# Performance work log

Measured on AMD Instinct MI355X. Metric: run time of the kernel, lower is better.

## Reference

```python
import jax, jax.numpy as jnp
import numpy as np


def setup_inputs() -> dict:
    key = jax.random.key(0)
    k1, k2, k3 = jax.random.split(key, 3)
    return {
        "x": jax.random.normal(k1, (1, 64, 28, 28), dtype=jnp.float32),
        "w1": jax.random.normal(k2, (128, 32, 3, 3, 2), dtype=jnp.float32),  # weights[0]
        "w2": jax.random.normal(k3, (64, 3, 2), dtype=jnp.float32),          # weights[1]
    }


def reference(x, w1, w2):
    # Stage 1: first unfold + einsum == depthwise size-3 conv along W (pad 1),
    # producing 2 taps (k) per channel.
    xr = x.reshape(64, 28, 28)                      # (j, m=H, n=W)
    xp = jnp.pad(xr, ((0, 0), (0, 0), (1, 1)))      # zero-pad W by 1
    # t3[j, m, i, n] = xp[j, m, n + i]  (i = kernel offset 0..2)
    t3 = jnp.stack([xp[:, :, i:i + 28] for i in range(3)], axis=2)  # (64,28,3,28)
    t4 = jnp.einsum('jmin,jik->jmnk', t3, w2)       # (64,28,28,2)

    # Stage 2: pairwise channel-sum 64 -> 32
    t5 = t4.reshape(32, 2, 28, 28, 2).sum(axis=1)   # (l=32, h=28, w=28, k=2)

    # Stage 3: the two remaining unfolds + final einsum == standard 3x3 conv,
    # pad 1, in_channels = (l,k) = 64, out_channels = 128.
    inp = jnp.transpose(t5, (0, 3, 1, 2)).reshape(1, 64, 28, 28)       # NCHW, C=(l,k)
    w = jnp.transpose(w1, (0, 1, 4, 2, 3)).reshape(128, 64, 3, 3)      # OIHW, I=(l,m)
    y = jax.lax.conv_general_dilated(
        inp, w, window_strides=(1, 1), padding=((1, 1), (1, 1)),
        dimension_numbers=('NCHW', 'OIHW', 'NCHW'))
    return y  # (1, 128, 28, 28)
```

## Files before the change

### kernel.cpp

```cpp
#include <hip/hip_runtime.h>
#include <hip/hip_bf16.h>

__global__ __launch_bounds__(256, 4) void fused_kernel(
    const float* __restrict__ x,
    const float* __restrict__ w1,
    const float* __restrict__ w2,
    float* __restrict__ y)
{
    __shared__ __align__(16) float sA[64 * 148];

    const int b     = blockIdx.x;
    const int opair = b / 14;
    const int band  = b % 14;
    const int tid   = threadIdx.x;

    {
        const int c  = tid >> 2;
        const int pr = tid & 3;
        const int m  = band * 2 + pr - 1;
        float* dst = &sA[c * 148 + pr * 36];
        if (m < 0 || m > 27) {
            #pragma unroll
            for (int t = 0; t < 7; ++t)
                ((float4*)dst)[t] = make_float4(0.f, 0.f, 0.f, 0.f);
            ((float2*)dst)[14] = make_float2(0.f, 0.f);
        } else {
            const int j0 = c & ~1;
            const int k  = c & 1;
            const float* xr0 = x + (j0 * 28 + m) * 28;
            const float* xr1 = xr0 + 28 * 28;
            const float* w2p = w2 + j0 * 6 + k;
            const float wa0 = w2p[0], wa1 = w2p[2],  wa2 = w2p[4];
            const float wb0 = w2p[6], wb1 = w2p[8],  wb2 = w2p[10];

            float4 pv0 = make_float4(0.f, 0.f, 0.f, 0.f);
            float4 pv1 = make_float4(0.f, 0.f, 0.f, 0.f);
            #pragma unroll
            for (int t = 0; t < 7; ++t) {
                float4 v0 = ((const float4*)xr0)[t];
                float4 v1 = ((const float4*)xr1)[t];
                float4 o;
                o.x = wa0 * pv0.z + wa1 * pv0.w + wa2 * v0.x
                    + wb0 * pv1.z + wb1 * pv1.w + wb2 * v1.x;
                o.y = wa0 * pv0.w + wa1 * v0.x + wa2 * v0.y
                    + wb0 * pv1.w + wb1 * v1.x + wb2 * v1.y;
                o.z = wa0 * v0.x + wa1 * v0.y + wa2 * v0.z
                    + wb0 * v1.x + wb1 * v1.y + wb2 * v1.z;
                o.w = wa0 * v0.y + wa1 * v0.z + wa2 * v0.w
                    + wb0 * v1.y + wb1 * v1.z + wb2 * v1.w;
                if (t == 0) o.x = 0.f;
                ((float4*)dst)[t] = o;
                pv0 = v0; pv1 = v1;
            }
            float t28 = wa0 * pv0.z + wa1 * pv0.w
                      + wb0 * pv1.z + wb1 * pv1.w;
            ((float2*)dst)[14] = make_float2(t28, 0.f);
        }
    }
    __syncthreads();

    const int oo    = tid >> 7;
    const int r     = tid & 127;
    const int c8    = r & 7;
    const int strip = r >> 3;
    const bool act  = (strip < 14);
    const int dh    = strip / 7;
    const int st    = strip % 7;
    const int o     = opair * 2 + oo;

    float acc0 = 0.f, acc1 = 0.f, acc2 = 0.f, acc3 = 0.f;
    if (act) {
        const float* wbo = w1 + o * 576;
        #pragma unroll 2
        for (int ci = 0; ci < 8; ++ci) {
            const int c = c8 + ci * 8;
            const float* wc = wbo + (c >> 1) * 18 + (c & 1);
            const float* sa = &sA[c * 148 + st * 4];
            #pragma unroll
            for (int dy = 0; dy < 3; ++dy) {
                const float w0  = wc[dy * 6 + 0];
                const float w1v = wc[dy * 6 + 2];
                const float w2v = wc[dy * 6 + 4];
                const float* row = sa + (dh + dy) * 36;
                float4 t0 = *(const float4*)row;
                float2 t1 = *(const float2*)(row + 4);
                acc0 += w0 * t0.x + w1v * t0.y + w2v * t0.z;
                acc1 += w0 * t0.y + w1v * t0.z + w2v * t0.w;
                acc2 += w0 * t0.z + w1v * t0.w + w2v * t1.x;
                acc3 += w0 * t0.w + w1v * t1.x + w2v * t1.y;
            }
        }
    }

    #pragma unroll
    for (int m = 1; m <= 4; m <<= 1) {
        acc0 += __shfl_xor(acc0, m);
        acc1 += __shfl_xor(acc1, m);
        acc2 += __shfl_xor(acc2, m);
        acc3 += __shfl_xor(acc3, m);
    }

    if (act && c8 == 0) {
        const int R = band * 2 + dh;
        float* yp = y + (o * 28 + R) * 28 + st * 4;
        *(float4*)yp = make_float4(acc0, acc1, acc2, acc3);
    }
}

extern "C" void kernel_launch(void* const* d_in, const int* in_sizes, int n_in,
                              void* d_out, int out_size, void* d_ws, size_t ws_size,
                              hipStream_t stream) {
    const float* x  = (const float*)d_in[0];
    const float* w1 = (const float*)d_in[1];
    const float* w2 = (const float*)d_in[2];
    float* yout = (float*)d_out;

    fused_kernel<<<dim3(896), dim3(256), 0, stream>>>(x, w1, w2, yout);
}
```

Baseline: 17.34 us.

## Enlarge row band per block to four output rows and pair channel taps

Each block now computes four output rows instead of two, so the stage-1 depthwise result (6 padded rows per channel) is built once for more outputs, which cuts the redundant halo recomputation. The grid is halved to 448 blocks. In stage 2 each thread handles both k taps of a channel group l, using float2 weight loads and a 4-way shuffle reduction instead of 8-way, and every lane in the 28 active strips does useful work. Shared memory per block grows and the launch bound drops to 2 blocks per SM, which lowers occupancy and parallelism.

```diff
diff --git a/kernel.cpp b/kernel.cpp
--- a/kernel.cpp
+++ b/kernel.cpp
@@ -1,24 +1,24 @@
 #include <hip/hip_runtime.h>
 #include <hip/hip_bf16.h>
 
-__global__ __launch_bounds__(256, 4) void fused_kernel(
+__global__ __launch_bounds__(256, 2) void fused_kernel(
     const float* __restrict__ x,
     const float* __restrict__ w1,
     const float* __restrict__ w2,
     float* __restrict__ y)
 {
-    __shared__ __align__(16) float sA[64 * 148];
+    __shared__ __align__(16) float sA[64 * 220];
 
     const int b     = blockIdx.x;
-    const int opair = b / 14;
-    const int band  = b % 14;
+    const int opair = b / 7;
+    const int band  = b % 7;
     const int tid   = threadIdx.x;
 
-    {
-        const int c  = tid >> 2;
-        const int pr = tid & 3;
-        const int m  = band * 2 + pr - 1;
-        float* dst = &sA[c * 148 + pr * 36];
+    for (int task = tid; task < 384; task += 256) {
+        const int c  = task / 6;
+        const int pr = task % 6;
+        const int m  = band * 4 + pr - 1;
+        float* dst = &sA[c * 220 + pr * 36];
         if (m < 0 || m > 27) {
             #pragma unroll
             for (int t = 0; t < 7; ++t)
@@ -61,47 +61,52 @@
 
     const int oo    = tid >> 7;
     const int r     = tid & 127;
-    const int c8    = r & 7;
-    const int strip = r >> 3;
-    const bool act  = (strip < 14);
-    const int dh    = strip / 7;
-    const int st    = strip % 7;
+    const int c4    = r & 3;
+    const int strip = r >> 2;
+    const bool act  = (strip < 28);
+    const int sclp  = act ? strip : 0;
+    const int dh    = sclp / 7;
+    const int st    = sclp % 7;
     const int o     = opair * 2 + oo;
 
     float acc0 = 0.f, acc1 = 0.f, acc2 = 0.f, acc3 = 0.f;
-    if (act) {
-        const float* wbo = w1 + o * 576;
-        #pragma unroll 2
-        for (int ci = 0; ci < 8; ++ci) {
-            const int c = c8 + ci * 8;
-            const float* wc = wbo + (c >> 1) * 18 + (c & 1);
-            const float* sa = &sA[c * 148 + st * 4];
-            #pragma unroll
-            for (int dy = 0; dy < 3; ++dy) {
-                const float w0  = wc[dy * 6 + 0];
-                const float w1v = wc[dy * 6 + 2];
-                const float w2v = wc[dy * 6 + 4];
-                const float* row = sa + (dh + dy) * 36;
-                float4 t0 = *(const float4*)row;
-                float2 t1 = *(const float2*)(row + 4);
-                acc0 += w0 * t0.x + w1v * t0.y + w2v * t0.z;
-                acc1 += w0 * t0.y + w1v * t0.z + w2v * t0.w;
-                acc2 += w0 * t0.z + w1v * t0.w + w2v * t1.x;
-                acc3 += w0 * t0.w + w1v * t1.x + w2v * t1.y;
-            }
+    const float* wbo = w1 + o * 576;
+
+    #pragma unroll 2
+    for (int li = 0; li < 8; ++li) {
+        const int l = c4 + li * 4;
+        const float* w9 = wbo + l * 18;
+        const float* rowA = &sA[(2 * l) * 220 + dh * 36 + st * 4];
+        #pragma unroll
+        for (int dy = 0; dy < 3; ++dy) {
+            float2 ws0 = *(const float2*)(w9 + dy * 6 + 0);
+            float2 ws1 = *(const float2*)(w9 + dy * 6 + 2);
+            float2 ws2 = *(const float2*)(w9 + dy * 6 + 4);
+            const float* rA = rowA + dy * 36;
+            const float* rB = rA + 220;
+            float4 a  = *(const float4*)rA;
+            float2 a2 = *(const float2*)(rA + 4);
+            float4 bb = *(const float4*)rB;
+            float2 b2 = *(const float2*)(rB + 4);
+
+            acc0 += ws0.x * a.x  + ws1.x * a.y  + ws2.x * a.z
+                  + ws0.y * bb.x + ws1.y * bb.y + ws2.y * bb.z;
+            acc1 += ws0.x * a.y  + ws1.x * a.z  + ws2.x * a.w
+                  + ws0.y * bb.y + ws1.y * bb.z + ws2.y * bb.w;
+            acc2 += ws0.x * a.z  + ws1.x * a.w  + ws2.x * a2.x
+                  + ws0.y * bb.z + ws1.y * bb.w + ws2.y * b2.x;
+            acc3 += ws0.x * a.w  + ws1.x * a2.x + ws2.x * a2.y
+                  + ws0.y * bb.w + ws1.y * b2.x + ws2.y * b2.y;
         }
     }
 
-    #pragma unroll
-    for (int m = 1; m <= 4; m <<= 1) {
-        acc0 += __shfl_xor(acc0, m);
-        acc1 += __shfl_xor(acc1, m);
-        acc2 += __shfl_xor(acc2, m);
-        acc3 += __shfl_xor(acc3, m);
-    }
+    acc0 += __shfl_xor(acc0, 1); acc1 += __shfl_xor(acc1, 1);
+    acc2 += __shfl_xor(acc2, 1); acc3 += __shfl_xor(acc3, 1);
+    acc0 += __shfl_xor(acc0, 2); acc1 += __shfl_xor(acc1, 2);
+    acc2 += __shfl_xor(acc2, 2); acc3 += __shfl_xor(acc3, 2);
 
-    if (act && c8 == 0) {
-        const int R = band * 2 + dh;
+    if (act && c4 == 0) {
+        const int R = band * 4 + dh;
         float* yp = y + (o * 28 + R) * 28 + st * 4;
         *(float4*)yp = make_float4(acc0, acc1, acc2, acc3);
     }
@@ -115,5 +120,5 @@
     const float* w2 = (const float*)d_in[2];
     float* yout = (float*)d_out;
 
-    fused_kernel<<<dim3(896), dim3(256), 0, stream>>>(x, w1, w2, yout);
+    fused_kernel<<<dim3(448), dim3(256), 0, stream>>>(x, w1, w2, yout);
 }
```

After: 14.71 us. 15.1% less time.

## Enlarge row band to four, preload weights in registers, drop idle threads

Applied to the files above, without the earlier changes.

Each block now covers four output rows instead of two, using 448 threads so every thread is active (the old layout left 32 of 128 threads per output idle). Each thread preloads its 72 w1 weights into registers with vectorized loads before the stage-1 compute, instead of issuing scalar strided global loads inside the inner loop. This halves the grid, reduces redundant recomputation of halo rows in stage 1, and overlaps the weight fetch with stage 1. In exchange register pressure rises, occupancy drops and the grid has fewer blocks.

```diff
diff --git a/kernel.cpp b/kernel.cpp
--- a/kernel.cpp
+++ b/kernel.cpp
@@ -1,24 +1,45 @@
 #include <hip/hip_runtime.h>
 #include <hip/hip_bf16.h>
 
-__global__ __launch_bounds__(256, 4) void fused_kernel(
+__global__ __launch_bounds__(448, 2) void fused_kernel(
     const float* __restrict__ x,
     const float* __restrict__ w1,
     const float* __restrict__ w2,
     float* __restrict__ y)
 {
-    __shared__ __align__(16) float sA[64 * 148];
+    __shared__ __align__(16) float sA[64 * 220];
 
     const int b     = blockIdx.x;
-    const int opair = b / 14;
-    const int band  = b % 14;
+    const int opair = b / 7;
+    const int band  = b % 7;
     const int tid   = threadIdx.x;
 
+    const int l8    = tid & 7;
+    const int strip = tid >> 3;
+    const int oo    = strip / 28;
+    const int rr    = strip % 28;
+    const int dh    = rr / 7;
+    const int st    = rr % 7;
+    const int o     = opair * 2 + oo;
+
+    float wl[4][18];
     {
-        const int c  = tid >> 2;
-        const int pr = tid & 3;
-        const int m  = band * 2 + pr - 1;
-        float* dst = &sA[c * 148 + pr * 36];
+        const float* wb = w1 + o * 576 + l8 * 18;
+        #pragma unroll
+        for (int li = 0; li < 4; ++li) {
+            const float* p = wb + li * 144;
+            #pragma unroll
+            for (int t = 0; t < 4; ++t)
+                *(float4*)&wl[li][t * 4] = *(const float4*)(p + t * 4);
+            *(float2*)&wl[li][16] = *(const float2*)(p + 16);
+        }
+    }
+
+    if (tid < 384) {
+        const int c  = tid / 6;
+        const int pr = tid % 6;
+        const int m  = band * 4 + pr - 1;
+        float* dst = &sA[c * 220 + pr * 36];
         if (m < 0 || m > 27) {
             #pragma unroll
             for (int t = 0; t < 7; ++t)
@@ -39,17 +60,17 @@
             for (int t = 0; t < 7; ++t) {
                 float4 v0 = ((const float4*)xr0)[t];
                 float4 v1 = ((const float4*)xr1)[t];
-                float4 o;
-                o.x = wa0 * pv0.z + wa1 * pv0.w + wa2 * v0.x
-                    + wb0 * pv1.z + wb1 * pv1.w + wb2 * v1.x;
-                o.y = wa0 * pv0.w + wa1 * v0.x + wa2 * v0.y
-                    + wb0 * pv1.w + wb1 * v1.x + wb2 * v1.y;
-                o.z = wa0 * v0.x + wa1 * v0.y + wa2 * v0.z
-                    + wb0 * v1.x + wb1 * v1.y + wb2 * v1.z;
-                o.w = wa0 * v0.y + wa1 * v0.z + wa2 * v0.w
-                    + wb0 * v1.y + wb1 * v1.z + wb2 * v1.w;
-                if (t == 0) o.x = 0.f;
-                ((float4*)dst)[t] = o;
+                float4 ov;
+                ov.x = wa0 * pv0.z + wa1 * pv0.w + wa2 * v0.x
+                     + wb0 * pv1.z + wb1 * pv1.w + wb2 * v1.x;
+                ov.y = wa0 * pv0.w + wa1 * v0.x + wa2 * v0.y
+                     + wb0 * pv1.w + wb1 * v1.x + wb2 * v1.y;
+                ov.z = wa0 * v0.x + wa1 * v0.y + wa2 * v0.z
+                     + wb0 * v1.x + wb1 * v1.y + wb2 * v1.z;
+                ov.w = wa0 * v0.y + wa1 * v0.z + wa2 * v0.w
+                     + wb0 * v1.y + wb1 * v1.z + wb2 * v1.w;
+                if (t == 0) ov.x = 0.f;
+                ((float4*)dst)[t] = ov;
                 pv0 = v0; pv1 = v1;
             }
             float t28 = wa0 * pv0.z + wa1 * pv0.w
@@ -59,35 +80,26 @@
     }
     __syncthreads();
 
-    const int oo    = tid >> 7;
-    const int r     = tid & 127;
-    const int c8    = r & 7;
-    const int strip = r >> 3;
-    const bool act  = (strip < 14);
-    const int dh    = strip / 7;
-    const int st    = strip % 7;
-    const int o     = opair * 2 + oo;
+    float acc0 = 0.f, acc1 = 0.f, acc2 = 0.f, acc3 = 0.f;
 
-    float acc0 = 0.f, acc1 = 0.f, acc2 = 0.f, acc3 = 0.f;
-    if (act) {
-        const float* wbo = w1 + o * 576;
-        #pragma unroll 2
-        for (int ci = 0; ci < 8; ++ci) {
-            const int c = c8 + ci * 8;
-            const float* wc = wbo + (c >> 1) * 18 + (c & 1);
-            const float* sa = &sA[c * 148 + st * 4];
+    #pragma unroll
+    for (int li = 0; li < 4; ++li) {
+        #pragma unroll
+        for (int ch = 0; ch < 2; ++ch) {
+            const int c = (l8 + li * 8) * 2 + ch;
+            const float* sa = &sA[c * 220 + dh * 36 + st * 4];
             #pragma unroll
             for (int dy = 0; dy < 3; ++dy) {
-                const float w0  = wc[dy * 6 + 0];
-                const float w1v = wc[dy * 6 + 2];
-                const float w2v = wc[dy * 6 + 4];
-                const float* row = sa + (dh + dy) * 36;
-                float4 t0 = *(const float4*)row;
-                float2 t1 = *(const float2*)(row + 4);
-                acc0 += w0 * t0.x + w1v * t0.y + w2v * t0.z;
-                acc1 += w0 * t0.y + w1v * t0.z + w2v * t0.w;
-                acc2 += w0 * t0.z + w1v * t0.w + w2v * t1.x;
-                acc3 += w0 * t0.w + w1v * t1.x + w2v * t1.y;
+                const float wa  = wl[li][dy * 6 + 0 + ch];
+                const float wbv = wl[li][dy * 6 + 2 + ch];
+                const float wc  = wl[li][dy * 6 + 4 + ch];
+                const float* rA = sa + dy * 36;
+                float4 t0 = *(const float4*)rA;
+                float2 t1 = *(const float2*)(rA + 4);
+                acc0 += wa * t0.x + wbv * t0.y + wc * t0.z;
+                acc1 += wa * t0.y + wbv * t0.z + wc * t0.w;
+                acc2 += wa * t0.z + wbv * t0.w + wc * t1.x;
+                acc3 += wa * t0.w + wbv * t1.x + wc * t1.y;
             }
         }
     }
@@ -100,8 +112,8 @@
         acc3 += __shfl_xor(acc3, m);
     }
 
-    if (act && c8 == 0) {
-        const int R = band * 2 + dh;
+    if (l8 == 0) {
+        const int R = band * 4 + dh;
         float* yp = y + (o * 28 + R) * 28 + st * 4;
         *(float4*)yp = make_float4(acc0, acc1, acc2, acc3);
     }
@@ -115,5 +127,5 @@
     const float* w2 = (const float*)d_in[2];
     float* yout = (float*)d_out;
 
-    fused_kernel<<<dim3(896), dim3(256), 0, stream>>>(x, w1, w2, yout);
+    fused_kernel<<<dim3(448), dim3(448), 0, stream>>>(x, w1, w2, yout);
 }
```

New measurement: 17.34 us. About the same (+0.0%).
